# Optimization experiments

Hardware: AMD Instinct MI355X
Metric: run time of the kernel (lower is better)

Reference implementation:

```python
import jax, jax.numpy as jnp
import numpy as np
from jax import lax

B, Z, X, Y = 8, 4, 32, 32
N = Z * X * Y
REAL_SIZE = jnp.array([25.0, 25.0, 4.0], dtype=jnp.float32)
THRESHOLD = 0.5
CUTOFF = 2.0


def setup_inputs() -> dict:
    key = jax.random.key(0)
    k1, k2 = jax.random.split(key)
    pred = jax.random.normal(k1, (B, Z, X, Y, 10), dtype=jnp.float32)
    targ = jax.random.uniform(k2, (B, Z, X, Y, 10), dtype=jnp.float32)
    return {"pred": pred, "targ": targ}


def _grid():
    z, x, y = jnp.meshgrid(jnp.arange(Z), jnp.arange(X), jnp.arange(Y), indexing="ij")
    return jnp.stack([z, x, y], -1).reshape(N, 3).astype(jnp.float32)


def _nms_mask(adj0, a0):
    # Fixed-size masked version of the original iterative suppression:
    # adj0: [N,N] bool, strictly-upper-triangular 'closer than cutoff' graph
    # a0:   [N] bool, currently active (above-threshold) points in conf-desc order
    def step(state):
        a, _ = state
        m = adj0 & a[:, None] & a[None, :]
        mf = m.astype(jnp.float32)
        r = mf.sum(0)                              # restrain_tensor = DIS.sum(0)
        r = r - (r != 0).astype(jnp.float32) @ mf  # subtract suppressed suppressors
        return ((r == 0.0) & a, a.sum())
    def cond(state):
        a, prev = state
        return a.sum() != prev
    a, _ = lax.while_loop(cond, step, (a0, jnp.int32(-1)))
    return a


def _per_batch(pd_conf, pd_pos, pd_R, tg_conf, tg_pos, tg_R):
    # pd_conf/tg_conf: [N]; pd_pos/tg_pos: [N,3] normalized; pd_R/tg_R: [N,3,3]
    pd_active = pd_conf > THRESHOLD
    tg_active = tg_conf > THRESHOLD
    # sort predictions by confidence descending, inactive pushed to the end
    skey = jnp.where(pd_active, pd_conf, -jnp.inf)
    order = jnp.argsort(-skey)
    pd_pos = pd_pos[order]
    pd_R = pd_R[order]
    a0 = pd_active[order]
    # NMS in NORMALIZED coordinates (as in the original module: real_size scaling
    # is applied only AFTER argnms)
    d = jnp.sqrt(jnp.sum((pd_pos[:, None, :] - pd_pos[None, :, :]) ** 2, -1))  # [N,N]
    iu = jnp.arange(N)
    adj0 = (d < CUTOFF) & (iu[:, None] < iu[None, :])
    keep = lax.stop_gradient(_nms_mask(adj0, a0))
    # greedy matching in real coordinates
    pd_r = pd_pos * REAL_SIZE
    tg_r = tg_pos * REAL_SIZE
    dist = jnp.sqrt(jnp.sum((tg_r[:, None, :] - pd_r[None, :, :]) ** 2, -1))  # [N_tg, N_pd]
    within = (dist < CUTOFF) & tg_active[:, None] & keep[None, :]
    has = within.any(0)                 # pred j has at least one target within cutoff
    first_tg = jnp.argmax(within, 0)    # first (lowest-index) matching target per pred
    tp = has.sum().astype(jnp.int32)
    n_pd = keep.sum().astype(jnp.int32)
    n_tg = tg_active.sum().astype(jnp.int32)
    cm = jnp.stack([tp, n_pd - tp, n_tg - tp])  # [matched, unmatched_pred, unmatched_targ]
    # mean rotation-angle error over matched pairs (3 rotation rows each)
    tgRm = tg_R[first_tg]  # [N,3,3]
    cos = jnp.sum(pd_R * tgRm, -1) / (
        jnp.linalg.norm(pd_R, axis=-1) * jnp.linalg.norm(tgRm, axis=-1))
    ang = jnp.arccos(jnp.clip(cos, -1.0, 1.0)) / jnp.pi * 180.0  # [N,3]
    w = has.astype(jnp.float32)[:, None]
    ms = jnp.where(tp > 0,
                   jnp.sum(ang * w) / (3.0 * jnp.maximum(tp, 1).astype(jnp.float32)),
                   0.0)
    return cm, ms


def _forward(pred, targ):
    grid = _grid()
    zxy = jnp.array([Z, X, Y], dtype=jnp.float32)
    def fields(t, is_pred):
        conf = jax.nn.sigmoid(t[..., 0]) if is_pred else t[..., 0]
        conf = conf.reshape(B, N)
        pos = (t[..., 1:4].reshape(B, N, 3) + grid) / zxy  # (off + cell_idx)/ZXY
        rx = t[..., 4:7].reshape(B, N, 3)
        ry = t[..., 7:10].reshape(B, N, 3)
        R = jnp.stack([rx, ry, jnp.cross(rx, ry)], axis=-2)  # [B,N,3,3]
        return conf, pos, R
    pc, pp, pR = fields(pred, True)
    tc, tpos, tR = fields(targ, False)
    cm, ms = jax.vmap(_per_batch)(pc, pp, pR, tc, tpos, tR)
    return cm.reshape(B, 1, 1, 3), ms.reshape(B, 1, 1, 1).astype(jnp.float32)


def reference(pred, targ):
    return _forward(pred, targ)
```

## Files before the change

### kernel.cpp

```cpp
#include <hip/hip_runtime.h>
#include <math.h>

#define NB    8
#define NPTS  4096
#define NTH   1024
#define SPT   4
#define NFILT 16
#define MAXQ  512
#define MAXU  256
#define MAXK  256

#define WS_PCC  0
#define WS_TCC  512
#define WS_PKEY 1024
#define WS_PPOS 263168
#define WS_TPOS 787456

__device__ __forceinline__ int blockReduceSumI(int v, int* scr, int tid) {
    #pragma unroll
    for (int o = 32; o > 0; o >>= 1) v += __shfl_down(v, o, 64);
    if ((tid & 63) == 0) scr[tid >> 6] = v;
    __syncthreads();
    if (tid == 0) {
        int s = 0;
        #pragma unroll
        for (int w = 0; w < NTH / 64; ++w) s += scr[w];
        scr[16] = s;
    }
    __syncthreads();
    return scr[16];
}

__device__ __forceinline__ float blockReduceSumF(float v, float* scr, int tid) {
    #pragma unroll
    for (int o = 32; o > 0; o >>= 1) v += __shfl_down(v, o, 64);
    if ((tid & 63) == 0) scr[tid >> 6] = v;
    __syncthreads();
    if (tid == 0) {
        float s = 0.0f;
        #pragma unroll
        for (int w = 0; w < NTH / 64; ++w) s += scr[w];
        scr[16] = s;
    }
    __syncthreads();
    return scr[16];
}

__device__ __forceinline__ float rowAngleDeg(float a0, float a1, float a2,
                                             float b0, float b1, float b2) {
    float dot = a0 * b0 + a1 * b1 + a2 * b2;
    float na = sqrtf(a0 * a0 + a1 * a1 + a2 * a2);
    float nb = sqrtf(b0 * b0 + b1 * b1 + b2 * b2);
    float c = dot / (na * nb);
    c = fminf(1.0f, fmaxf(-1.0f, c));
    return acosf(c) * 57.29577951308232f;
}

__global__ __launch_bounds__(256) void prep_kernel(const float* __restrict__ pred,
                                                   const float* __restrict__ targ,
                                                   unsigned char* __restrict__ ws) {
    __shared__ int wcnt[4];
    unsigned int* pcc = (unsigned int*)(ws + WS_PCC);
    unsigned int* tcc = (unsigned int*)(ws + WS_TCC);
    unsigned long long* pkey = (unsigned long long*)(ws + WS_PKEY);
    float4* ppos = (float4*)(ws + WS_PPOS);
    float4* tpos = (float4*)(ws + WS_TPOS);

    const int tid = threadIdx.x;
    const int blk = blockIdx.x;
    const int tensor = blk >> 7;
    const int batch = (blk >> 4) & 7;
    const int chunk = blk & 15;
    const int n = chunk * 256 + tid;
    const float* base = (tensor ? targ : pred)
                        + (size_t)batch * NPTS * 10 + (size_t)n * 10;
    float2 f0 = *(const float2*)base;
    float2 f1 = *(const float2*)(base + 2);
    float gz = (float)(n >> 10);
    float gx = (float)((n >> 5) & 31);
    float gy = (float)(n & 31);

    bool active;
    unsigned long long key = 0;
    float4 rec;
    if (tensor == 0) {
        float conf = 1.0f / (1.0f + expf(-f0.x));
        active = conf > 0.5f;
        unsigned int u = ~(__float_as_uint(conf) | 0x80000000u);
        key = ((unsigned long long)u << 32) | (unsigned int)n;
        rec = make_float4((f0.y + gz) * 0.25f,
                          (f1.x + gx) * 0.03125f,
                          (f1.y + gy) * 0.03125f,
                          (float)n);
    } else {
        active = f0.x > 0.5f;
        rec = make_float4((f0.y + gz) * 0.25f * 25.0f,
                          (f1.x + gx) * 0.03125f * 25.0f,
                          (f1.y + gy) * 0.03125f * 4.0f,
                          (float)n);
    }

    const int lane = tid & 63, wid = tid >> 6;
    unsigned long long ball = __ballot(active);
    int lofs = __popcll(ball & ((1ull << lane) - 1ull));
    if (lane == 0) wcnt[wid] = __popcll(ball);
    __syncthreads();
    int wb = 0;
    for (int w = 0; w < wid; ++w) wb += wcnt[w];
    if (tid == 0) {
        unsigned int t = (unsigned int)(wcnt[0] + wcnt[1] + wcnt[2] + wcnt[3]);
        (tensor ? tcc : pcc)[batch * 16 + chunk] = t;
    }
    if (active) {
        int e = batch * NPTS + chunk * 256 + wb + lofs;
        if (tensor == 0) { pkey[e] = key; ppos[e] = rec; }
        else tpos[e] = rec;
    }
}

__global__ __launch_bounds__(NTH) void molan_kernel(const float* __restrict__ pred,
                                                    const float* __restrict__ targ,
                                                    const unsigned char* __restrict__ ws,
                                                    float* __restrict__ out) {
    __shared__ int   scr_i[32];
    __shared__ float scr_f[32];
    __shared__ int   cnt[4];
    __shared__ int   ccP[16], ccT[16];
    __shared__ unsigned long long f_key[NFILT];
    __shared__ float f_x[NFILT], f_y[NFILT], f_z[NFILT];
    __shared__ unsigned long long q_key[MAXQ];
    __shared__ float q_x[MAXQ], q_y[MAXQ], q_z[MAXQ];
    __shared__ int   q_res[MAXQ];
    __shared__ unsigned long long u_key[MAXU];
    __shared__ float u_x[MAXU], u_y[MAXU], u_z[MAXU];
    __shared__ float k_x[MAXK], k_y[MAXK], k_z[MAXK];
    __shared__ int   k_idx[MAXK];
    __shared__ unsigned int k_match[MAXK];

    const int b = blockIdx.x;
    const int tid = threadIdx.x;
    const float* pb = pred + (size_t)b * NPTS * 10;
    const float* tb = targ + (size_t)b * NPTS * 10;
    const unsigned long long* pkey = (const unsigned long long*)(ws + WS_PKEY) + b * NPTS;
    const float4* ppos = (const float4*)(ws + WS_PPOS) + b * NPTS;
    const float4* tpos = (const float4*)(ws + WS_TPOS) + b * NPTS;

    if (tid < 16) ccP[tid] = (int)((const unsigned int*)(ws + WS_PCC))[b * 16 + tid];
    else if (tid < 32) ccT[tid - 16] = (int)((const unsigned int*)(ws + WS_TCC))[b * 16 + tid - 16];
    __syncthreads();

    unsigned long long key[SPT];
    bool  act[SPT];
    int   pidx[SPT];
    float cx[SPT], cy[SPT], cz[SPT];
    #pragma unroll
    for (int s = 0; s < SPT; ++s) {
        int slot = tid + NTH * s;
        bool a = (slot & 255) < ccP[slot >> 8];
        act[s] = a;
        key[s] = ~0ull;
        cx[s] = cy[s] = cz[s] = 0.f; pidx[s] = 0;
        if (a) {
            key[s] = pkey[slot];
            float4 p = ppos[slot];
            cx[s] = p.x; cy[s] = p.y; cz[s] = p.z; pidx[s] = (int)p.w;
        }
    }
    bool  t_act[SPT];
    int   t_n[SPT];
    float t_x[SPT], t_y[SPT], t_z[SPT];
    #pragma unroll
    for (int s = 0; s < SPT; ++s) {
        int slot = tid + NTH * s;
        bool a = (slot & 255) < ccT[slot >> 8];
        t_act[s] = a;
        t_x[s] = t_y[s] = t_z[s] = 0.f; t_n[s] = 0;
        if (a) {
            float4 p = tpos[slot];
            t_x[s] = p.x; t_y[s] = p.y; t_z[s] = p.z; t_n[s] = (int)p.w;
        }
    }

    int loc = 0;
    #pragma unroll
    for (int s = 0; s < SPT; ++s) loc += act[s] ? 1 : 0;
    int cur = blockReduceSumI(loc, scr_i, tid);
    int prev = -1;
    while (cur != prev) {
        {
            unsigned long long bk = ~0ull;
            float bx = 0.f, by = 0.f, bz = 0.f;
            #pragma unroll
            for (int s = 0; s < SPT; ++s)
                if (act[s] && key[s] < bk) { bk = key[s]; bx = cx[s]; by = cy[s]; bz = cz[s]; }
            #pragma unroll
            for (int o = 32; o > 0; o >>= 1) {
                unsigned long long ok = __shfl_xor(bk, o, 64);
                float ox = __shfl_xor(bx, o, 64);
                float oy = __shfl_xor(by, o, 64);
                float oz = __shfl_xor(bz, o, 64);
                if (ok < bk) { bk = ok; bx = ox; by = oy; bz = oz; }
            }
            if ((tid & 63) == 0) {
                int w = tid >> 6;
                f_key[w] = bk; f_x[w] = bx; f_y[w] = by; f_z[w] = bz;
            }
        }
        __syncthreads();

        bool sflag[SPT], pend[SPT];
        #pragma unroll
        for (int s = 0; s < SPT; ++s) {
            sflag[s] = false; pend[s] = false;
            if (!act[s]) continue;
            bool found = false;
            for (int f = 0; f < NFILT; ++f) {
                if (f_key[f] < key[s]) {
                    float dx = f_x[f] - cx[s], dy = f_y[f] - cy[s], dz = f_z[f] - cz[s];
                    if (dx * dx + dy * dy + dz * dz < 4.0f) { found = true; break; }
                }
            }
            if (found) sflag[s] = true;
            else pend[s] = true;
        }
        do {
            if (tid == 0) cnt[1] = 0;
            __syncthreads();
            int qe[SPT];
            #pragma unroll
            for (int s = 0; s < SPT; ++s) {
                qe[s] = -1;
                if (pend[s]) {
                    int e = atomicAdd(&cnt[1], 1);
                    if (e < MAXQ) {
                        q_key[e] = key[s]; q_x[e] = cx[s]; q_y[e] = cy[s]; q_z[e] = cz[s];
                        q_res[e] = 0;
                        qe[s] = e; pend[s] = false;
                    }
                }
            }
            __syncthreads();
            const int Q = min(cnt[1], MAXQ);
            for (int e = 0; e < Q; ++e) {
                unsigned long long qk = q_key[e];
                float qx = q_x[e], qy = q_y[e], qz = q_z[e];
                bool hit = false;
                #pragma unroll
                for (int s = 0; s < SPT; ++s) {
                    if (act[s] && key[s] < qk) {
                        float dx = cx[s] - qx, dy = cy[s] - qy, dz = cz[s] - qz;
                        if (dx * dx + dy * dy + dz * dz < 4.0f) hit = true;
                    }
                }
                if (hit) q_res[e] = 1;
            }
            __syncthreads();
            #pragma unroll
            for (int s = 0; s < SPT; ++s)
                if (qe[s] >= 0) sflag[s] = (q_res[qe[s]] != 0);
        } while (cnt[1] > MAXQ);

        bool upend[SPT], supp[SPT];
        #pragma unroll
        for (int s = 0; s < SPT; ++s) {
            upend[s] = act[s] && !sflag[s];
            supp[s] = false;
        }
        do {
            if (tid == 0) cnt[2] = 0;
            __syncthreads();
            #pragma unroll
            for (int s = 0; s < SPT; ++s) {
                if (upend[s]) {
                    int e = atomicAdd(&cnt[2], 1);
                    if (e < MAXU) {
                        u_key[e] = key[s]; u_x[e] = cx[s]; u_y[e] = cy[s]; u_z[e] = cz[s];
                        upend[s] = false;
                    }
                }
            }
            __syncthreads();
            const int Ku = min(cnt[2], MAXU);
            #pragma unroll
            for (int s = 0; s < SPT; ++s) {
                if (!act[s] || supp[s]) continue;
                for (int e = 0; e < Ku; ++e) {
                    if (u_key[e] < key[s]) {
                        float dx = u_x[e] - cx[s], dy = u_y[e] - cy[s], dz = u_z[e] - cz[s];
                        if (dx * dx + dy * dy + dz * dz < 4.0f) { supp[s] = true; break; }
                    }
                }
            }
        } while (cnt[2] > MAXU);
        loc = 0;
        #pragma unroll
        for (int s = 0; s < SPT; ++s) {
            if (act[s] && supp[s]) act[s] = false;
            loc += act[s] ? 1 : 0;
        }
        prev = cur;
        cur = blockReduceSumI(loc, scr_i, tid);
    }
    const int n_pd = cur;

    bool kpend[SPT];
    #pragma unroll
    for (int s = 0; s < SPT; ++s) kpend[s] = act[s];
    int loc_tp = 0;
    float loc_ang = 0.0f;
    do {
        if (tid == 0) cnt[3] = 0;
        __syncthreads();
        #pragma unroll
        for (int s = 0; s < SPT; ++s) {
            if (kpend[s]) {
                int e = atomicAdd(&cnt[3], 1);
                if (e < MAXK) {
                    k_x[e] = cx[s] * 25.0f; k_y[e] = cy[s] * 25.0f; k_z[e] = cz[s] * 4.0f;
                    k_idx[e] = pidx[s];
                    k_match[e] = 0xFFFFFFFFu;
                    kpend[s] = false;
                }
            }
        }
        __syncthreads();
        const int K = min(cnt[3], MAXK);
        #pragma unroll
        for (int s = 0; s < SPT; ++s) {
            if (!t_act[s]) continue;
            float tx = t_x[s], ty = t_y[s], tz = t_z[s];
            for (int e = 0; e < K; ++e) {
                float dx = tx - k_x[e], dy = ty - k_y[e], dz = tz - k_z[e];
                if (dx * dx + dy * dy + dz * dz < 4.0f)
                    atomicMin(&k_match[e], (unsigned int)t_n[s]);
            }
        }
        __syncthreads();
        if (tid < K) {
            unsigned int m = k_match[tid];
            if (m != 0xFFFFFFFFu) {
                ++loc_tp;
                const float2* pr = (const float2*)(pb + (size_t)k_idx[tid] * 10 + 4);
                float2 p0 = pr[0], p1 = pr[1], p2v = pr[2];
                float ax0 = p0.x, ax1 = p0.y, ax2 = p1.x;
                float ay0 = p1.y, ay1 = p2v.x, ay2 = p2v.y;
                float az0 = ax1 * ay2 - ax2 * ay1;
                float az1 = ax2 * ay0 - ax0 * ay2;
                float az2 = ax0 * ay1 - ax1 * ay0;
                const float2* tr = (const float2*)(tb + (size_t)m * 10 + 4);
                float2 t0 = tr[0], t1 = tr[1], t2v = tr[2];
                float bx0 = t0.x, bx1 = t0.y, bx2 = t1.x;
                float by0 = t1.y, by1 = t2v.x, by2 = t2v.y;
                float bz0 = bx1 * by2 - bx2 * by1;
                float bz1 = bx2 * by0 - bx0 * by2;
                float bz2 = bx0 * by1 - bx1 * by0;
                loc_ang += rowAngleDeg(ax0, ax1, ax2, bx0, bx1, bx2);
                loc_ang += rowAngleDeg(ay0, ay1, ay2, by0, by1, by2);
                loc_ang += rowAngleDeg(az0, az1, az2, bz0, bz1, bz2);
            }
        }
    } while (cnt[3] > MAXK);

    int tp = blockReduceSumI(loc_tp, scr_i, tid);
    float angsum = blockReduceSumF(loc_ang, scr_f, tid);

    if (tid == 0) {
        int nt = 0;
        #pragma unroll
        for (int i = 0; i < 16; ++i) nt += ccT[i];
        out[b * 3 + 0] = (float)tp;
        out[b * 3 + 1] = (float)(n_pd - tp);
        out[b * 3 + 2] = (float)(nt - tp);
        out[NB * 3 + b] = (tp > 0) ? (angsum / (3.0f * (float)tp)) : 0.0f;
    }
}

extern "C" void kernel_launch(void* const* d_in, const int* in_sizes, int n_in,
                              void* d_out, int out_size, void* d_ws, size_t ws_size,
                              hipStream_t stream) {
    const float* pred = (const float*)d_in[0];
    const float* targ = (const float*)d_in[1];
    float* out = (float*)d_out;
    unsigned char* ws = (unsigned char*)d_ws;
    prep_kernel<<<dim3(256), dim3(256), 0, stream>>>(pred, targ, ws);
    molan_kernel<<<dim3(NB), dim3(NTH), 0, stream>>>(pred, targ, ws, out);
}
```

Baseline: 76.69 us.

## Fuse prep kernel into main kernel, reading raw inputs directly per batch

```diff
diff --git a/kernel.cpp b/kernel.cpp
--- a/kernel.cpp
+++ b/kernel.cpp
@@ -10,12 +10,6 @@
 #define MAXU  256
 #define MAXK  256
 
-#define WS_PCC  0
-#define WS_TCC  512
-#define WS_PKEY 1024
-#define WS_PPOS 263168
-#define WS_TPOS 787456
-
 __device__ __forceinline__ int blockReduceSumI(int v, int* scr, int tid) {
     #pragma unroll
     for (int o = 32; o > 0; o >>= 1) v += __shfl_down(v, o, 64);
@@ -56,76 +50,12 @@
     return acosf(c) * 57.29577951308232f;
 }
 
-__global__ __launch_bounds__(256) void prep_kernel(const float* __restrict__ pred,
+__global__ __launch_bounds__(NTH) void molan_fused(const float* __restrict__ pred,
                                                    const float* __restrict__ targ,
-                                                   unsigned char* __restrict__ ws) {
-    __shared__ int wcnt[4];
-    unsigned int* pcc = (unsigned int*)(ws + WS_PCC);
-    unsigned int* tcc = (unsigned int*)(ws + WS_TCC);
-    unsigned long long* pkey = (unsigned long long*)(ws + WS_PKEY);
-    float4* ppos = (float4*)(ws + WS_PPOS);
-    float4* tpos = (float4*)(ws + WS_TPOS);
-
-    const int tid = threadIdx.x;
-    const int blk = blockIdx.x;
-    const int tensor = blk >> 7;
-    const int batch = (blk >> 4) & 7;
-    const int chunk = blk & 15;
-    const int n = chunk * 256 + tid;
-    const float* base = (tensor ? targ : pred)
-                        + (size_t)batch * NPTS * 10 + (size_t)n * 10;
-    float2 f0 = *(const float2*)base;
-    float2 f1 = *(const float2*)(base + 2);
-    float gz = (float)(n >> 10);
-    float gx = (float)((n >> 5) & 31);
-    float gy = (float)(n & 31);
-
-    bool active;
-    unsigned long long key = 0;
-    float4 rec;
-    if (tensor == 0) {
-        float conf = 1.0f / (1.0f + expf(-f0.x));
-        active = conf > 0.5f;
-        unsigned int u = ~(__float_as_uint(conf) | 0x80000000u);
-        key = ((unsigned long long)u << 32) | (unsigned int)n;
-        rec = make_float4((f0.y + gz) * 0.25f,
-                          (f1.x + gx) * 0.03125f,
-                          (f1.y + gy) * 0.03125f,
-                          (float)n);
-    } else {
-        active = f0.x > 0.5f;
-        rec = make_float4((f0.y + gz) * 0.25f * 25.0f,
-                          (f1.x + gx) * 0.03125f * 25.0f,
-                          (f1.y + gy) * 0.03125f * 4.0f,
-                          (float)n);
-    }
-
-    const int lane = tid & 63, wid = tid >> 6;
-    unsigned long long ball = __ballot(active);
-    int lofs = __popcll(ball & ((1ull << lane) - 1ull));
-    if (lane == 0) wcnt[wid] = __popcll(ball);
-    __syncthreads();
-    int wb = 0;
-    for (int w = 0; w < wid; ++w) wb += wcnt[w];
-    if (tid == 0) {
-        unsigned int t = (unsigned int)(wcnt[0] + wcnt[1] + wcnt[2] + wcnt[3]);
-        (tensor ? tcc : pcc)[batch * 16 + chunk] = t;
-    }
-    if (active) {
-        int e = batch * NPTS + chunk * 256 + wb + lofs;
-        if (tensor == 0) { pkey[e] = key; ppos[e] = rec; }
-        else tpos[e] = rec;
-    }
-}
-
-__global__ __launch_bounds__(NTH) void molan_kernel(const float* __restrict__ pred,
-                                                    const float* __restrict__ targ,
-                                                    const unsigned char* __restrict__ ws,
-                                                    float* __restrict__ out) {
+                                                   float* __restrict__ out) {
     __shared__ int   scr_i[32];
     __shared__ float scr_f[32];
     __shared__ int   cnt[4];
-    __shared__ int   ccP[16], ccT[16];
     __shared__ unsigned long long f_key[NFILT];
     __shared__ float f_x[NFILT], f_y[NFILT], f_z[NFILT];
     __shared__ unsigned long long q_key[MAXQ];
@@ -141,49 +71,43 @@
     const int tid = threadIdx.x;
     const float* pb = pred + (size_t)b * NPTS * 10;
     const float* tb = targ + (size_t)b * NPTS * 10;
-    const unsigned long long* pkey = (const unsigned long long*)(ws + WS_PKEY) + b * NPTS;
-    const float4* ppos = (const float4*)(ws + WS_PPOS) + b * NPTS;
-    const float4* tpos = (const float4*)(ws + WS_TPOS) + b * NPTS;
-
-    if (tid < 16) ccP[tid] = (int)((const unsigned int*)(ws + WS_PCC))[b * 16 + tid];
-    else if (tid < 32) ccT[tid - 16] = (int)((const unsigned int*)(ws + WS_TCC))[b * 16 + tid - 16];
-    __syncthreads();
 
     unsigned long long key[SPT];
     bool  act[SPT];
-    int   pidx[SPT];
     float cx[SPT], cy[SPT], cz[SPT];
+    bool  t_act[SPT];
+    float t_x[SPT], t_y[SPT], t_z[SPT];
+    int loc = 0, loc_t = 0;
     #pragma unroll
     for (int s = 0; s < SPT; ++s) {
-        int slot = tid + NTH * s;
-        bool a = (slot & 255) < ccP[slot >> 8];
+        const int n = tid + NTH * s;
+        const float2* p2 = (const float2*)(pb + (size_t)n * 10);
+        const float2* t2 = (const float2*)(tb + (size_t)n * 10);
+        float2 f0 = p2[0];
+        float2 f1 = p2[1];
+        float2 g0 = t2[0];
+        float2 g1 = t2[1];
+        const float gz = (float)(n >> 10);
+        const float gx = (float)((n >> 5) & 31);
+        const float gy = (float)(n & 31);
+        float conf = 1.0f / (1.0f + expf(-f0.x));
+        bool a = conf > 0.5f;
         act[s] = a;
-        key[s] = ~0ull;
-        cx[s] = cy[s] = cz[s] = 0.f; pidx[s] = 0;
-        if (a) {
-            key[s] = pkey[slot];
-            float4 p = ppos[slot];
-            cx[s] = p.x; cy[s] = p.y; cz[s] = p.z; pidx[s] = (int)p.w;
-        }
-    }
-    bool  t_act[SPT];
-    int   t_n[SPT];
-    float t_x[SPT], t_y[SPT], t_z[SPT];
-    #pragma unroll
-    for (int s = 0; s < SPT; ++s) {
-        int slot = tid + NTH * s;
-        bool a = (slot & 255) < ccT[slot >> 8];
-        t_act[s] = a;
-        t_x[s] = t_y[s] = t_z[s] = 0.f; t_n[s] = 0;
-        if (a) {
-            float4 p = tpos[slot];
-            t_x[s] = p.x; t_y[s] = p.y; t_z[s] = p.z; t_n[s] = (int)p.w;
-        }
-    }
-
-    int loc = 0;
-    #pragma unroll
-    for (int s = 0; s < SPT; ++s) loc += act[s] ? 1 : 0;
+        loc += a ? 1 : 0;
+        unsigned int u = ~(__float_as_uint(conf) | 0x80000000u);
+        key[s] = a ? (((unsigned long long)u << 32) | (unsigned int)n)
+                   : ~0ull;
+        cx[s] = (f0.y + gz) * 0.25f;
+        cy[s] = (f1.x + gx) * 0.03125f;
+        cz[s] = (f1.y + gy) * 0.03125f;
+        bool ta = g0.x > 0.5f;
+        t_act[s] = ta;
+        loc_t += ta ? 1 : 0;
+        t_x[s] = (g0.y + gz) * 6.25f;
+        t_y[s] = (g1.x + gx) * 0.78125f;
+        t_z[s] = (g1.y + gy) * 0.125f;
+    }
+
     int cur = blockReduceSumI(loc, scr_i, tid);
     int prev = -1;
     while (cur != prev) {
@@ -317,7 +241,7 @@
                 int e = atomicAdd(&cnt[3], 1);
                 if (e < MAXK) {
                     k_x[e] = cx[s] * 25.0f; k_y[e] = cy[s] * 25.0f; k_z[e] = cz[s] * 4.0f;
-                    k_idx[e] = pidx[s];
+                    k_idx[e] = tid + NTH * s;
                     k_match[e] = 0xFFFFFFFFu;
                     kpend[s] = false;
                 }
@@ -332,7 +256,7 @@
             for (int e = 0; e < K; ++e) {
                 float dx = tx - k_x[e], dy = ty - k_y[e], dz = tz - k_z[e];
                 if (dx * dx + dy * dy + dz * dz < 4.0f)
-                    atomicMin(&k_match[e], (unsigned int)t_n[s]);
+                    atomicMin(&k_match[e], (unsigned int)(tid + NTH * s));
             }
         }
         __syncthreads();
@@ -363,11 +287,9 @@
 
     int tp = blockReduceSumI(loc_tp, scr_i, tid);
     float angsum = blockReduceSumF(loc_ang, scr_f, tid);
+    int nt = blockReduceSumI(loc_t, scr_i, tid);
 
     if (tid == 0) {
-        int nt = 0;
-        #pragma unroll
-        for (int i = 0; i < 16; ++i) nt += ccT[i];
         out[b * 3 + 0] = (float)tp;
         out[b * 3 + 1] = (float)(n_pd - tp);
         out[b * 3 + 2] = (float)(nt - tp);
@@ -381,7 +303,6 @@
     const float* pred = (const float*)d_in[0];
     const float* targ = (const float*)d_in[1];
     float* out = (float*)d_out;
-    unsigned char* ws = (unsigned char*)d_ws;
-    prep_kernel<<<dim3(256), dim3(256), 0, stream>>>(pred, targ, ws);
-    molan_kernel<<<dim3(NB), dim3(NTH), 0, stream>>>(pred, targ, ws, out);
-}
+    (void)d_ws; (void)ws_size;
+    molan_fused<<<dim3(NB), dim3(NTH), 0, stream>>>(pred, targ, out);
+}
```

New measurement: 72.67 us. 5.2% less time.
